# Kernel tuning notes

Hardware: AMD Instinct MI355X
Metric: run time of the kernel (lower is better)

## Reference

```python
import jax, jax.numpy as jnp
import numpy as np

B = 4096
D = 64  # emb_dim, hardcoded in UserEmb/ItemEmb


def setup_inputs() -> dict:
    key = jax.random.key(0)
    ks = jax.random.split(key, 26)
    n = lambda k, shape, s=1.0: jax.random.normal(k, shape, dtype=jnp.float32) * s
    inp = {
        'user_emb': jax.random.randint(ks[0], (B, 4), 0, 6, dtype=jnp.int32),
        'item_emb': jax.random.randint(ks[1], (B, 10242), 0, 2, dtype=jnp.int32),
        'edge_emb': jnp.zeros((B,), dtype=jnp.int32),  # edges_emb has num_embeddings=1
        # UserEmb params
        'gender_tab': n(ks[2], (98, D)),
        'age_tab': n(ks[3], (7, D)),
        'occ_tab': n(ks[4], (21, D)),
        'area_tab': n(ks[5], (3402, D)),
        'user_W': n(ks[6], (4 * D, D), 0.05),  # stored [in,out]
        'user_b': n(ks[7], (D,), 0.05),
        # ItemEmb params
        'rate_tab': n(ks[8], (6, D)),
        'genre_W': n(ks[9], (25, D), 0.05),
        'director_W': n(ks[10], (2186, D), 0.02),
        'actor_W': n(ks[11], (8030, D), 0.01),
        'item_W': n(ks[12], (4 * D, D), 0.05),
        'item_b': n(ks[13], (D,), 0.05),
        # GLNFeat params (torch: randn * 0.5)
        'edges_tab': n(ks[14], (1, D)),
        'uu_w': n(ks[15], (D,), 0.5),
        'ui_w': n(ks[16], (D,), 0.5),
        'iu_w': n(ks[17], (D,), 0.5),
        'ii_w': n(ks[18], (D,), 0.5),
        'edge_W': n(ks[19], (D, D), 0.5),
        'uu_W1': n(ks[20], (D, D), 0.5),
        'ui_W1': n(ks[21], (D, D), 0.5),
        'iu_W1': n(ks[22], (D, D), 0.5),
        'ii_W1': n(ks[23], (D, D), 0.5),
    }
    return inp


def _lrelu(v):
    return jnp.where(v >= 0, v, 0.01 * v)  # nn.LeakyReLU default slope


def reference(user_emb, item_emb, edge_emb, gender_tab, age_tab, occ_tab, area_tab,
              user_W, user_b, rate_tab, genre_W, director_W, actor_W, item_W, item_b,
              edges_tab, uu_w, ui_w, iu_w, ii_w, edge_W, uu_W1, ui_W1, iu_W1, ii_W1):
    a = 0.12
    b = 0.12
    # UserEmb
    u_cat = jnp.concatenate([gender_tab[user_emb[:, 0]], age_tab[user_emb[:, 1]],
                             occ_tab[user_emb[:, 2]], area_tab[user_emb[:, 3]]], axis=1)
    x = (u_cat @ user_W + user_b) * a  # [B, D]
    # ItemEmb: multi-hot fields projected then mean-normalized by count
    genre = item_emb[:, 1:26].astype(jnp.float32)
    director = item_emb[:, 26:2212].astype(jnp.float32)
    actor = item_emb[:, 2212:10242].astype(jnp.float32)
    ge = (genre @ genre_W) / jnp.sum(genre, 1, keepdims=True)
    de = (director @ director_W) / jnp.sum(director, 1, keepdims=True)
    ae = (actor @ actor_W) / jnp.sum(actor, 1, keepdims=True)
    i_cat = jnp.concatenate([rate_tab[item_emb[:, 0]], ge, de, ae], axis=1)
    y = (i_cat @ item_W + item_b) * a  # [B, D]
    edge = edges_tab[edge_emb] * b  # [B, D]

    def outer_mm(u, v, M):
        # stop_gradient(outer(u, v) @ M) == u[:,None] * (v @ M), avoids [B,B]
        return jax.lax.stop_gradient(u[:, None] * (v @ M))

    xe = x * edge
    ye = y * edge
    x_xx = xe @ uu_w      # [B]
    x_xy_x = xe @ ui_w
    x_xy_y = ye @ ui_w
    t1 = outer_mm(x_xx, x_xx, x)
    t2 = outer_mm(x_xy_x, x_xy_y, y)
    x_buy = (_lrelu(t1 @ uu_W1) + _lrelu(t2 @ ui_W1)) / 2
    y_yy = ye @ ii_w
    y_yx_y = ye @ iu_w
    y_yx_x = xe @ iu_w
    t3 = outer_mm(y_yy, y_yy, y)
    t4 = outer_mm(y_yx_y, y_yx_x, x)
    y_buy = (_lrelu(t3 @ ii_W1) + _lrelu(t4 @ iu_W1)) / 2
    new = _lrelu(edge @ edge_W)
    return ((x_buy + x) / 2, (y_buy + y) / 2, (new + edge) / 2)
```

## Files before the change

### kernel.cpp

```cpp
#include <hip/hip_runtime.h>
#include <cstddef>

constexpr int BATCH = 4096;
constexpr int ITEM_COLS = 10242;
constexpr int FBTK = 10304;
constexpr int NPART = 15;

constexpr int R_GENDER = 0;
constexpr int R_AGE    = 98;
constexpr int R_OCC    = 105;
constexpr int R_AREA   = 126;
constexpr int R_RATE   = 3528;
constexpr int R_FU     = 3534;

constexpr size_t OFF_FU  = 0;
constexpr size_t OFF_NEW = OFF_FU + (size_t)R_FU * 64;
constexpr size_t OFF_FBT = OFF_NEW + 64;
constexpr size_t OFF_X   = OFF_FBT + (size_t)64 * FBTK / 2;
constexpr size_t OFF_Y   = OFF_X + (size_t)BATCH * 64;
constexpr size_t OFF_P   = OFF_Y + (size_t)BATCH * 64;
constexpr size_t OFF_C   = OFF_P + (size_t)NPART * BATCH * 64;
constexpr size_t OFF_S   = OFF_C + (size_t)NPART * BATCH;
constexpr size_t OFF_SC  = OFF_S + 4ull * 64;

__device__ const int AST[NPART] = {0, 24, 792, 1560, 2208, 2976, 3744, 4512, 5280, 6048, 6816, 7584, 8352, 9120, 9888};
__device__ const int VS [NPART] = {0, 25, 792, 1560, 2211, 2976, 3744, 4512, 5280, 6048, 6816, 7584, 8352, 9120, 9888};
__device__ const int VE [NPART] = {25, 792, 1560, 2211, 2976, 3744, 4512, 5280, 6048, 6816, 7584, 8352, 9120, 9888, 10241};
__device__ const int PLEN[NPART] = {128, 768, 768, 768, 768, 768, 768, 768, 768, 768, 768, 768, 768, 768, 384};

typedef __attribute__((ext_vector_type(8))) short bf16x8;
typedef __attribute__((ext_vector_type(4))) float f32x4;

__device__ __forceinline__ float lrelu(float v) { return v >= 0.0f ? v : 0.01f * v; }

__device__ __forceinline__ unsigned bf_rne_pair(float lo, float hi) {
    unsigned ul = __builtin_bit_cast(unsigned, lo);
    unsigned uh = __builtin_bit_cast(unsigned, hi);
    ul += 0x7fffu + ((ul >> 16) & 1u);
    uh += 0x7fffu + ((uh >> 16) & 1u);
    return (ul >> 16) | (uh & 0xffff0000u);
}

__global__ __launch_bounds__(256) void k_fuse(
        const float* __restrict__ gender_tab, const float* __restrict__ age_tab,
        const float* __restrict__ occ_tab, const float* __restrict__ area_tab,
        const float* __restrict__ user_W, const float* __restrict__ rate_tab,
        const float* __restrict__ genre_W, const float* __restrict__ director_W,
        const float* __restrict__ actor_W, const float* __restrict__ item_W,
        const float* __restrict__ edges_tab, const float* __restrict__ edge_W,
        float* __restrict__ Fu, float* __restrict__ NEWt, short* __restrict__ Fbt,
        float* __restrict__ S) {
    const int t = threadIdx.x;
    const int bx = blockIdx.x;
    if (bx == 0) S[t] = 0.0f;
    if (bx < 884) {
        int n = t & 63;
        int rb = __builtin_amdgcn_readfirstlane(t >> 6);
        int r = bx * 4 + rb;
        if (r > R_FU) return;
        if (r == R_FU) {
            float acc = 0.0f;
#pragma unroll
            for (int k = 0; k < 64; ++k)
                acc = fmaf(edges_tab[k] * 0.12f, edge_W[k * 64 + n], acc);
            NEWt[n] = lrelu(acc);
            return;
        }
        const float* src;
        const float* W;
        if (r < R_AGE)       { src = gender_tab + (size_t)r * 64;            W = user_W;            }
        else if (r < R_OCC)  { src = age_tab    + (size_t)(r - R_AGE) * 64;  W = user_W + 64 * 64;  }
        else if (r < R_AREA) { src = occ_tab    + (size_t)(r - R_OCC) * 64;  W = user_W + 128 * 64; }
        else if (r < R_RATE) { src = area_tab   + (size_t)(r - R_AREA) * 64; W = user_W + 192 * 64; }
        else                 { src = rate_tab   + (size_t)(r - R_RATE) * 64; W = item_W;            }
        float acc = 0.0f;
#pragma unroll
        for (int k = 0; k < 64; ++k)
            acc = fmaf(src[k], W[k * 64 + n], acc);
        Fu[(size_t)r * 64 + n] = acc;
        return;
    }
    const int KT0 = (bx - 884) * 64;
    const int n = t & 63;
    const int rb = __builtin_amdgcn_readfirstlane(t >> 6);
    __shared__ float T[64 * 65];
    for (int rl = 0; rl < 16; ++rl) {
        int r = rl * 4 + rb;
        int KT = KT0 + r;
        float acc = 0.0f;
        if (KT < 10241) {
            const float* src;
            const float* W;
            if (KT < 25)        { src = genre_W    + (size_t)KT * 64;          W = item_W + 64 * 64;  }
            else if (KT < 2211) { src = director_W + (size_t)(KT - 25) * 64;   W = item_W + 128 * 64; }
            else                { src = actor_W    + (size_t)(KT - 2211) * 64; W = item_W + 192 * 64; }
#pragma unroll
            for (int k = 0; k < 64; ++k)
                acc = fmaf(src[k], W[k * 64 + n], acc);
        }
        T[r * 65 + n] = acc;
    }
    __syncthreads();
    int n2 = t >> 2, sg = t & 3;
    unsigned dw[8];
#pragma unroll
    for (int d = 0; d < 8; ++d)
        dw[d] = bf_rne_pair(T[(sg * 16 + 2 * d) * 65 + n2], T[(sg * 16 + 2 * d + 1) * 65 + n2]);
    uint4* dst = (uint4*)(Fbt + (size_t)n2 * FBTK + KT0 + sg * 16);
    dst[0] = make_uint4(dw[0], dw[1], dw[2], dw[3]);
    dst[1] = make_uint4(dw[4], dw[5], dw[6], dw[7]);
}

__global__ __launch_bounds__(256) void k_item(const int* __restrict__ item,
                                              const short* __restrict__ Fbt,
                                              float* __restrict__ P, float* __restrict__ C) {
    const int part = blockIdx.y;
    const int ast = AST[part], vs = VS[part], ve = VE[part], len = PLEN[part];
    const int m0 = blockIdx.x * 64;
    const int t = threadIdx.x;
    const int lane = t & 63;
    const int w = __builtin_amdgcn_readfirstlane(t >> 6);
    const int q = lane >> 4, r16 = lane & 15;
    const int m = m0 + w * 16 + r16;
    const int* __restrict__ arow = item + (size_t)m * ITEM_COLS + 1;

    f32x4 acc[5];
#pragma unroll
    for (int s = 0; s < 5; ++s) acc[s] = (f32x4){0.f, 0.f, 0.f, 0.f};

    const short o = (r16 == 0) ? (short)0x3f80 : (short)0;
    const bf16x8 ones = {o, o, o, o, o, o, o, o};

    for (int kb = 0; kb < len; kb += 128) {
        const int K0 = ast + kb;
        int va[4][8];
        if (K0 >= vs && K0 + 128 <= ve) {
#pragma unroll
            for (int kt = 0; kt < 4; ++kt) {
                const int* p = arow + K0 + kt * 32 + q * 8;
#pragma unroll
                for (int j = 0; j < 8; ++j) va[kt][j] = p[j];
            }
        } else {
#pragma unroll
            for (int kt = 0; kt < 4; ++kt) {
#pragma unroll
                for (int j = 0; j < 8; ++j) {
                    int KT = K0 + kt * 32 + q * 8 + j;
                    int KTc = KT > 10240 ? 10240 : KT;
                    int v = arow[KTc];
                    va[kt][j] = (KT >= vs && KT < ve) ? v : 0;
                }
            }
        }
#pragma unroll
        for (int kt = 0; kt < 4; ++kt) {
            bf16x8 a;
#pragma unroll
            for (int j = 0; j < 8; ++j) a[j] = va[kt][j] ? (short)0x3f80 : (short)0;
            const short* fb = Fbt + K0 + kt * 32 + q * 8;
#pragma unroll
            for (int s = 0; s < 4; ++s) {
                bf16x8 b = *(const bf16x8*)(fb + (size_t)(s * 16 + r16) * FBTK);
                acc[s] = __builtin_amdgcn_mfma_f32_16x16x32_bf16(a, b, acc[s], 0, 0, 0);
            }
            acc[4] = __builtin_amdgcn_mfma_f32_16x16x32_bf16(a, ones, acc[4], 0, 0, 0);
        }
    }
    const size_t pb = (size_t)part * BATCH + m0 + w * 16 + q * 4;
#pragma unroll
    for (int reg = 0; reg < 4; ++reg) {
        float* pr = P + (pb + reg) * 64 + r16;
        pr[0] = acc[0][reg];
        pr[16] = acc[1][reg];
        pr[32] = acc[2][reg];
        pr[48] = acc[3][reg];
    }
    if (r16 == 0) {
#pragma unroll
        for (int reg = 0; reg < 4; ++reg)
            C[(size_t)part * BATCH + m0 + w * 16 + q * 4 + reg] = acc[4][reg];
    }
}

__device__ __forceinline__ float wred(float v) {
#pragma unroll
    for (int m = 1; m < 64; m <<= 1) v += __shfl_xor(v, m, 64);
    return v;
}

__global__ __launch_bounds__(256) void k_mid(const int* __restrict__ item, const int* __restrict__ edge_emb,
                                             const int* __restrict__ user_emb,
                                             const float* __restrict__ Fu, const float* __restrict__ user_b,
                                             const float* __restrict__ P, const float* __restrict__ C,
                                             const float* __restrict__ item_b, const float* __restrict__ edges_tab,
                                             const float* __restrict__ uu_w, const float* __restrict__ ui_w,
                                             const float* __restrict__ iu_w, const float* __restrict__ ii_w,
                                             float* __restrict__ X, float* __restrict__ Y,
                                             float* __restrict__ SC, float* __restrict__ S) {
    const int t = threadIdx.x;
    const int n = t & 63;
    const int wv = __builtin_amdgcn_readfirstlane(t >> 6);
    const float uuw = uu_w[n], uiw = ui_w[n], iuw = iu_w[n], iiw = ii_w[n];
    const float ib = item_b[n], ub = user_b[n];
    const size_t cs = (size_t)BATCH * 64;
    float s1 = 0.0f, s2 = 0.0f, s3 = 0.0f, s4 = 0.0f;

    for (int i = 0; i < 4; ++i) {
        int b = blockIdx.x * 16 + wv * 4 + i;
        const int* ue = user_emb + (size_t)b * 4;
        float x = (Fu[(size_t)(R_GENDER + ue[0]) * 64 + n]
                 + Fu[(size_t)(R_AGE    + ue[1]) * 64 + n]
                 + Fu[(size_t)(R_OCC    + ue[2]) * 64 + n]
                 + Fu[(size_t)(R_AREA   + ue[3]) * 64 + n] + ub) * 0.12f;
        X[(size_t)b * 64 + n] = x;
        int ri = item[(size_t)b * ITEM_COLS];
        size_t base = (size_t)b * 64 + n;
        float sg = P[base], cg = C[b];
        float sd = 0.0f, cd = 0.0f, sa = 0.0f, ca = 0.0f;
#pragma unroll
        for (int p2 = 1; p2 < 4; ++p2)  { sd += P[base + p2 * cs]; cd += C[p2 * BATCH + b]; }
#pragma unroll
        for (int p2 = 4; p2 < 15; ++p2) { sa += P[base + p2 * cs]; ca += C[p2 * BATCH + b]; }
        float y = (Fu[(size_t)(R_RATE + ri) * 64 + n] + sg / cg + sd / cd + sa / ca + ib) * 0.12f;
        Y[(size_t)b * 64 + n] = y;
        float e = edges_tab[(size_t)edge_emb[b] * 64 + n] * 0.12f;
        float xe = x * e, ye = y * e;
        float r1 = wred(xe * uuw);
        float r2 = wred(xe * uiw);
        float r3 = wred(xe * iuw);
        float r4 = wred(ye * uiw);
        float r5 = wred(ye * iiw);
        float r6 = wred(ye * iuw);
        if (n == 0) {
            SC[b] = r1; SC[BATCH + b] = r2; SC[2 * BATCH + b] = r5; SC[3 * BATCH + b] = r6;
        }
        s1 = fmaf(r1, x, s1);
        s2 = fmaf(r4, y, s2);
        s3 = fmaf(r5, y, s3);
        s4 = fmaf(r3, x, s4);
    }
    __shared__ float sp[4][4][64];
    sp[wv][0][n] = s1; sp[wv][1][n] = s2; sp[wv][2][n] = s3; sp[wv][3][n] = s4;
    __syncthreads();
    int i2 = t >> 6;
    float v = sp[0][i2][n] + sp[1][i2][n] + sp[2][i2][n] + sp[3][i2][n];
    atomicAdd(&S[i2 * 64 + n], v);
}

__global__ __launch_bounds__(256) void k_out(const float* __restrict__ X, const float* __restrict__ Y,
                                             const float* __restrict__ SC, const float* __restrict__ S,
                                             const float* __restrict__ uu_W1, const float* __restrict__ ui_W1,
                                             const float* __restrict__ iu_W1, const float* __restrict__ ii_W1,
                                             const float* __restrict__ NEWt, const float* __restrict__ edges_tab,
                                             const int* __restrict__ edge_emb, float* __restrict__ out) {
    const int t = threadIdx.x;
    const int n = t & 63, i = t >> 6;
    __shared__ float sS[4][64], sPB[4][64];
    sS[i][n] = S[i * 64 + n];
    __syncthreads();
    const float* W1 = (i == 0) ? uu_W1 : (i == 1) ? ui_W1 : (i == 2) ? ii_W1 : iu_W1;
    float p = 0.0f;
#pragma unroll
    for (int k = 0; k < 64; ++k) p = fmaf(sS[i][k], W1[k * 64 + n], p);
    sPB[i][n] = p;
    __syncthreads();
    const float p1 = sPB[0][n], p2 = sPB[1][n], p3 = sPB[2][n], p4 = sPB[3][n];
    const float nw = NEWt[n];
    for (int ii = 0; ii < 4; ++ii) {
        int b = blockIdx.x * 16 + i * 4 + ii;
        float xx = SC[b], xyx = SC[BATCH + b], yy = SC[2 * BATCH + b], yxy = SC[3 * BATCH + b];
        float x = X[(size_t)b * 64 + n], y = Y[(size_t)b * 64 + n];
        float o1 = ((lrelu(xx * p1) + lrelu(xyx * p2)) * 0.5f + x) * 0.5f;
        float o2 = ((lrelu(yy * p3) + lrelu(yxy * p4)) * 0.5f + y) * 0.5f;
        float e = edges_tab[(size_t)edge_emb[b] * 64 + n] * 0.12f;
        float o3 = (nw + e) * 0.5f;
        out[(size_t)b * 64 + n] = o1;
        out[((size_t)BATCH + b) * 64 + n] = o2;
        out[((size_t)2 * BATCH + b) * 64 + n] = o3;
    }
}

extern "C" void kernel_launch(void* const* d_in, const int* in_sizes, int n_in,
                              void* d_out, int out_size, void* d_ws, size_t ws_size,
                              hipStream_t stream) {
    (void)in_sizes; (void)n_in; (void)out_size; (void)ws_size;
    const int*   user_emb   = (const int*)  d_in[0];
    const int*   item_emb   = (const int*)  d_in[1];
    const int*   edge_emb   = (const int*)  d_in[2];
    const float* gender_tab = (const float*)d_in[3];
    const float* age_tab    = (const float*)d_in[4];
    const float* occ_tab    = (const float*)d_in[5];
    const float* area_tab   = (const float*)d_in[6];
    const float* user_W     = (const float*)d_in[7];
    const float* user_b     = (const float*)d_in[8];
    const float* rate_tab   = (const float*)d_in[9];
    const float* genre_W    = (const float*)d_in[10];
    const float* director_W = (const float*)d_in[11];
    const float* actor_W    = (const float*)d_in[12];
    const float* item_W     = (const float*)d_in[13];
    const float* item_b     = (const float*)d_in[14];
    const float* edges_tab  = (const float*)d_in[15];
    const float* uu_w       = (const float*)d_in[16];
    const float* ui_w       = (const float*)d_in[17];
    const float* iu_w       = (const float*)d_in[18];
    const float* ii_w       = (const float*)d_in[19];
    const float* edge_W     = (const float*)d_in[20];
    const float* uu_W1      = (const float*)d_in[21];
    const float* ui_W1      = (const float*)d_in[22];
    const float* iu_W1      = (const float*)d_in[23];
    const float* ii_W1      = (const float*)d_in[24];

    float* ws   = (float*)d_ws;
    float* Fu   = ws + OFF_FU;
    float* NEWt = ws + OFF_NEW;
    short* Fbt  = (short*)(ws + OFF_FBT);
    float* X    = ws + OFF_X;
    float* Y    = ws + OFF_Y;
    float* P    = ws + OFF_P;
    float* C    = ws + OFF_C;
    float* S    = ws + OFF_S;
    float* SC   = ws + OFF_SC;
    float* out  = (float*)d_out;

    hipLaunchKernelGGL(k_fuse, dim3(884 + FBTK / 64), dim3(256), 0, stream,
                       gender_tab, age_tab, occ_tab, area_tab, user_W, rate_tab,
                       genre_W, director_W, actor_W, item_W, edges_tab, edge_W, Fu, NEWt, Fbt, S);
    hipLaunchKernelGGL(k_item, dim3(BATCH / 64, NPART), dim3(256), 0, stream, item_emb, Fbt, P, C);
    hipLaunchKernelGGL(k_mid, dim3(BATCH / 16), dim3(256), 0, stream,
                       item_emb, edge_emb, user_emb, Fu, user_b, P, C, item_b, edges_tab,
                       uu_w, ui_w, iu_w, ii_w, X, Y, SC, S);
    hipLaunchKernelGGL(k_out, dim3(BATCH / 16), dim3(256), 0, stream,
                       X, Y, SC, S, uu_W1, ui_W1, iu_W1, ii_W1, NEWt, edges_tab, edge_emb, out);
}
```

Before: 360.9 us.

## Pre-pack multi-hot item matrix into bitmasks before the MFMA item kernel

Adds a k_pack kernel that reads each item row once and compresses the int32 multi-hot columns into bit masks using wave ballots. k_item then loads bytes from the packed buffer instead of re-reading 32-bit ints, shrinking its global memory traffic by about 32x. The cost is an extra kernel launch plus one full pass over the large int matrix. k_item's loads also become byte-granular and less coalesced.

```diff
diff --git a/kernel.cpp b/kernel.cpp
--- a/kernel.cpp
+++ b/kernel.cpp
@@ -5,6 +5,8 @@
 constexpr int ITEM_COLS = 10242;
 constexpr int FBTK = 10304;
 constexpr int NPART = 15;
+constexpr int PK_STRIDE_DW = 384;
+constexpr int PK_STRIDE_B  = 1536;
 
 constexpr int R_GENDER = 0;
 constexpr int R_AGE    = 98;
@@ -22,6 +24,7 @@
 constexpr size_t OFF_C   = OFF_P + (size_t)NPART * BATCH * 64;
 constexpr size_t OFF_S   = OFF_C + (size_t)NPART * BATCH;
 constexpr size_t OFF_SC  = OFF_S + 4ull * 64;
+constexpr size_t OFF_PK  = OFF_SC + 4ull * BATCH;
 
 __device__ const int AST[NPART] = {0, 24, 792, 1560, 2208, 2976, 3744, 4512, 5280, 6048, 6816, 7584, 8352, 9120, 9888};
 __device__ const int VS [NPART] = {0, 25, 792, 1560, 2211, 2976, 3744, 4512, 5280, 6048, 6816, 7584, 8352, 9120, 9888};
@@ -111,7 +114,30 @@
     dst[1] = make_uint4(dw[4], dw[5], dw[6], dw[7]);
 }
 
-__global__ __launch_bounds__(256) void k_item(const int* __restrict__ item,
+__global__ __launch_bounds__(256) void k_pack(const int* __restrict__ item,
+                                              unsigned* __restrict__ pk) {
+    const int t = threadIdx.x;
+    const int lane = t & 63;
+    const int chunk = blockIdx.x * 4 + (t >> 6);
+    const int row = chunk / 6, span = chunk - row * 6;
+    const int E0 = span * 2048;
+    const int* __restrict__ arow = item + (size_t)row * ITEM_COLS + 1;
+    unsigned long long kept = 0;
+#pragma unroll
+    for (int it = 0; it < 32; ++it) {
+        int KT = E0 + it * 64 + lane;
+        int KTc = KT > 10240 ? 10240 : KT;
+        int v = arow[KTc];
+        unsigned long long m = __ballot(KT <= 10240 && v != 0);
+        kept = (lane == it) ? m : kept;
+    }
+    if (lane < 32) {
+        unsigned* dst = pk + (size_t)row * PK_STRIDE_DW + span * 64 + lane * 2;
+        *(uint2*)dst = make_uint2((unsigned)kept, (unsigned)(kept >> 32));
+    }
+}
+
+__global__ __launch_bounds__(256) void k_item(const unsigned char* __restrict__ pkb,
                                               const short* __restrict__ Fbt,
                                               float* __restrict__ P, float* __restrict__ C) {
     const int part = blockIdx.y;
@@ -122,7 +148,7 @@
     const int w = __builtin_amdgcn_readfirstlane(t >> 6);
     const int q = lane >> 4, r16 = lane & 15;
     const int m = m0 + w * 16 + r16;
-    const int* __restrict__ arow = item + (size_t)m * ITEM_COLS + 1;
+    const unsigned char* __restrict__ prow = pkb + (size_t)m * PK_STRIDE_B;
 
     f32x4 acc[5];
 #pragma unroll
@@ -133,31 +159,27 @@
 
     for (int kb = 0; kb < len; kb += 128) {
         const int K0 = ast + kb;
-        int va[4][8];
-        if (K0 >= vs && K0 + 128 <= ve) {
-#pragma unroll
-            for (int kt = 0; kt < 4; ++kt) {
-                const int* p = arow + K0 + kt * 32 + q * 8;
-#pragma unroll
-                for (int j = 0; j < 8; ++j) va[kt][j] = p[j];
-            }
-        } else {
-#pragma unroll
-            for (int kt = 0; kt < 4; ++kt) {
+        unsigned bv[4];
+#pragma unroll
+        for (int kt = 0; kt < 4; ++kt)
+            bv[kt] = prow[(K0 >> 3) + kt * 4 + q];
+        const bool interior = (K0 >= vs) && (K0 + 128 <= ve);
+#pragma unroll
+        for (int kt = 0; kt < 4; ++kt) {
+            bf16x8 a;
+            if (interior) {
+#pragma unroll
+                for (int j = 0; j < 8; ++j)
+                    a[j] = ((bv[kt] >> j) & 1u) ? (short)0x3f80 : (short)0;
+            } else {
+                int kbase = K0 + kt * 32 + q * 8;
 #pragma unroll
                 for (int j = 0; j < 8; ++j) {
-                    int KT = K0 + kt * 32 + q * 8 + j;
-                    int KTc = KT > 10240 ? 10240 : KT;
-                    int v = arow[KTc];
-                    va[kt][j] = (KT >= vs && KT < ve) ? v : 0;
+                    bool bit = (bv[kt] >> j) & 1u;
+                    bool vld = (kbase + j >= vs) && (kbase + j < ve);
+                    a[j] = (bit && vld) ? (short)0x3f80 : (short)0;
                 }
             }
-        }
-#pragma unroll
-        for (int kt = 0; kt < 4; ++kt) {
-            bf16x8 a;
-#pragma unroll
-            for (int j = 0; j < 8; ++j) a[j] = va[kt][j] ? (short)0x3f80 : (short)0;
             const short* fb = Fbt + K0 + kt * 32 + q * 8;
 #pragma unroll
             for (int s = 0; s < 4; ++s) {
@@ -321,12 +343,15 @@
     float* C    = ws + OFF_C;
     float* S    = ws + OFF_S;
     float* SC   = ws + OFF_SC;
+    unsigned* PK = (unsigned*)(ws + OFF_PK);
     float* out  = (float*)d_out;
 
     hipLaunchKernelGGL(k_fuse, dim3(884 + FBTK / 64), dim3(256), 0, stream,
                        gender_tab, age_tab, occ_tab, area_tab, user_W, rate_tab,
                        genre_W, director_W, actor_W, item_W, edges_tab, edge_W, Fu, NEWt, Fbt, S);
-    hipLaunchKernelGGL(k_item, dim3(BATCH / 64, NPART), dim3(256), 0, stream, item_emb, Fbt, P, C);
+    hipLaunchKernelGGL(k_pack, dim3(BATCH * 6 / 4), dim3(256), 0, stream, item_emb, PK);
+    hipLaunchKernelGGL(k_item, dim3(BATCH / 64, NPART), dim3(256), 0, stream,
+                       (const unsigned char*)PK, Fbt, P, C);
     hipLaunchKernelGGL(k_mid, dim3(BATCH / 16), dim3(256), 0, stream,
                        item_emb, edge_emb, user_emb, Fu, user_b, P, C, item_b, edges_tab,
                        uu_w, ui_w, iu_w, ii_w, X, Y, SC, S);
```

Result: slower. 377.0 us (+4.5%).

## Coalesce multi-hot item loads via row-wise reads and ballot bitmasks

Applied to the files above, without the earlier changes.

The item kernel now reads the int32 multi-hot matrix row by row: each wavefront lane loads a consecutive column, which makes the global loads fully coalesced. A ballot over the wave packs each row segment into a 64-bit mask. The masks are then redistributed with shuffles to build the bf16 A-fragments for the MFMA. This removes the strided per-lane 8-element row loads, at the cost of 32 ballots and a few shuffles per 128-column step.

```diff
diff --git a/kernel.cpp b/kernel.cpp
--- a/kernel.cpp
+++ b/kernel.cpp
@@ -121,8 +121,8 @@
     const int lane = t & 63;
     const int w = __builtin_amdgcn_readfirstlane(t >> 6);
     const int q = lane >> 4, r16 = lane & 15;
-    const int m = m0 + w * 16 + r16;
-    const int* __restrict__ arow = item + (size_t)m * ITEM_COLS + 1;
+    const int mw = m0 + w * 16;
+    const int* __restrict__ ibase = item + (size_t)mw * ITEM_COLS + 1;
 
     f32x4 acc[5];
 #pragma unroll
@@ -133,31 +133,25 @@
 
     for (int kb = 0; kb < len; kb += 128) {
         const int K0 = ast + kb;
-        int va[4][8];
-        if (K0 >= vs && K0 + 128 <= ve) {
-#pragma unroll
-            for (int kt = 0; kt < 4; ++kt) {
-                const int* p = arow + K0 + kt * 32 + q * 8;
-#pragma unroll
-                for (int j = 0; j < 8; ++j) va[kt][j] = p[j];
-            }
-        } else {
-#pragma unroll
-            for (int kt = 0; kt < 4; ++kt) {
-#pragma unroll
-                for (int j = 0; j < 8; ++j) {
-                    int KT = K0 + kt * 32 + q * 8 + j;
-                    int KTc = KT > 10240 ? 10240 : KT;
-                    int v = arow[KTc];
-                    va[kt][j] = (KT >= vs && KT < ve) ? v : 0;
-                }
-            }
+        unsigned klo = 0, khi = 0;
+#pragma unroll
+        for (int it = 0; it < 32; ++it) {
+            const int rl = it >> 1, h = it & 1;
+            int KT = K0 + h * 64 + lane;
+            int KTc = KT > 10240 ? 10240 : KT;
+            int v = ibase[(size_t)rl * ITEM_COLS + KTc];
+            unsigned long long m = __ballot(v != 0 && KT >= vs && KT < ve);
+            klo = (lane == it) ? (unsigned)m : klo;
+            khi = (lane == it) ? (unsigned)(m >> 32) : khi;
         }
 #pragma unroll
         for (int kt = 0; kt < 4; ++kt) {
+            unsigned word = __shfl((kt & 1) ? khi : klo, r16 * 2 + (kt >> 1), 64);
+            unsigned byte = (word >> (q * 8)) & 0xffu;
             bf16x8 a;
 #pragma unroll
-            for (int j = 0; j < 8; ++j) a[j] = va[kt][j] ? (short)0x3f80 : (short)0;
+            for (int j = 0; j < 8; ++j)
+                a[j] = ((byte >> j) & 1u) ? (short)0x3f80 : (short)0;
             const short* fb = Fbt + K0 + kt * 32 + q * 8;
 #pragma unroll
             for (int s = 0; s < 4; ++s) {
@@ -167,7 +161,7 @@
             acc[4] = __builtin_amdgcn_mfma_f32_16x16x32_bf16(a, ones, acc[4], 0, 0, 0);
         }
     }
-    const size_t pb = (size_t)part * BATCH + m0 + w * 16 + q * 4;
+    const size_t pb = (size_t)part * BATCH + mw + q * 4;
 #pragma unroll
     for (int reg = 0; reg < 4; ++reg) {
         float* pr = P + (pb + reg) * 64 + r16;
@@ -179,7 +173,7 @@
     if (r16 == 0) {
 #pragma unroll
         for (int reg = 0; reg < 4; ++reg)
-            C[(size_t)part * BATCH + m0 + w * 16 + q * 4 + reg] = acc[4][reg];
+            C[(size_t)part * BATCH + mw + q * 4 + reg] = acc[4][reg];
     }
 }
 
```

Measured after the change: 361.7 us. Within noise of the previous version (+0.2%).
